# Kernel tuning notes

Hardware: AMD Instinct MI355X
Metric: run time of the kernel (lower is better)

Reference implementation:

```python
import jax, jax.numpy as jnp
import numpy as np

MODEL_DIM = 1024
NUM_EXPERTS = 64
CAPACITY_FACTOR = 1.0
MIN_CAPACITY = 8


def setup_inputs() -> dict:
    key = jax.random.key(0)
    kx, kw = jax.random.split(key)
    x = jax.random.normal(kx, (4, 2048, MODEL_DIM), dtype=jnp.float32)
    wg = jax.random.normal(kw, (MODEL_DIM, NUM_EXPERTS), dtype=jnp.float32) * (1.0 / np.sqrt(MODEL_DIM))
    return {"x": x, "wg": wg}


def reference(x, wg):
    d = x.shape[-1]
    tokens = x.reshape(-1, d)                      # [s, m]
    s = tokens.shape[0]
    e = wg.shape[1]
    # capacity per _capacity(): ceil(num_tokens/num_experts * capacity_factor), floored at min_capacity
    capacity = max(int(np.ceil(s / e * CAPACITY_FACTOR)), MIN_CAPACITY)

    logits = tokens @ wg                           # [s, e]  (wg Linear, no bias)
    gates = jax.nn.softmax(logits, axis=1)         # [s, e]

    indices1_s = jnp.argmax(gates, axis=1)         # [s] top-1 expert per token
    mask1 = jax.nn.one_hot(indices1_s, e, dtype=jnp.int32)  # [s, e]
    exp_counts = jnp.sum(mask1, axis=0)            # [e]

    # load-balancing aux loss
    me = jnp.mean(gates, axis=0)                   # [e]
    ce = jnp.mean(mask1.astype(jnp.float32), axis=0)
    l_aux = jnp.sum(me * ce) * e

    # position of each token within its expert's buffer
    locations1 = jnp.cumsum(mask1, axis=0) - 1     # [s, e]
    locations1_s = jnp.sum(locations1 * mask1, axis=1)  # [s]

    gates_masked = gates * mask1.astype(jnp.float32)    # [s, e]
    # one_hot zeros out indices >= capacity (token dropped)
    locations1_sc = jax.nn.one_hot(locations1_s, capacity, dtype=jnp.float32)  # [s, c]
    combine_weights = jnp.einsum('se,sc->sec', gates_masked, locations1_sc)    # [s, e, c]
    dispatch_mask = combine_weights.astype(bool)
    return (l_aux, combine_weights, dispatch_mask, mask1, exp_counts, indices1_s)
```

## Files before the change

kernel.cpp:

```cpp
#include <hip/hip_runtime.h>
#include <hip/hip_bf16.h>

#define S_TOK 8192
#define NEXP 64
#define MDIM 1024
#define CAP 128
#define BLK_TOK 32
#define NCH 256

#define OFF2 67108865
#define OFF3 134217729
#define OFF4 134742017
#define OFF5 134742081

__global__ __launch_bounds__(256) void gate_kernel(
    const float* __restrict__ x, const float* __restrict__ wg,
    unsigned char* __restrict__ ind, unsigned char* __restrict__ rnk,
    float* __restrict__ gval, unsigned char* __restrict__ counts,
    float* __restrict__ gparts)
{
  __shared__ float wgt[4 * 64 * NEXP];
  __shared__ float g_all[BLK_TOK][NEXP];
  __shared__ int s_ind[BLK_TOK];
  const int b = blockIdx.x;
  const int tid = threadIdx.x;
  const int lane = tid & 63;
  const int wv = tid >> 6;
  const int eg = lane & 15;
  const int tg = lane >> 4;
  const int tokbase = b * BLK_TOK + tg * 8;

  const float4* x4 = reinterpret_cast<const float4*>(x);
  const float4* wg4 = reinterpret_cast<const float4*>(wg);
  float4* wgt4 = reinterpret_cast<float4*>(wgt);

  float4 acc[8];
#pragma unroll
  for (int j = 0; j < 8; ++j) acc[j] = make_float4(0.f, 0.f, 0.f, 0.f);

#pragma unroll
  for (int p = 0; p < 4; ++p) {
    __syncthreads();
#pragma unroll
    for (int k = 0; k < 16; ++k) {
      const int c = k * 256 + tid;
      const int wq = c >> 10;
      const int rem = c & 1023;
      wgt4[c] = wg4[wq * 4096 + p * 1024 + rem];
    }
    __syncthreads();

    const float4* wrow = wgt4 + wv * 1024;
    const int xcol0 = wv * 64 + p * 16;
#pragma unroll 2
    for (int dq = 0; dq < 16; ++dq) {
      const float4 w0 = wrow[(4 * dq + 0) * 16 + eg];
      const float4 w1 = wrow[(4 * dq + 1) * 16 + eg];
      const float4 w2 = wrow[(4 * dq + 2) * 16 + eg];
      const float4 w3 = wrow[(4 * dq + 3) * 16 + eg];
#pragma unroll
      for (int j = 0; j < 8; ++j) {
        const float4 xv = x4[(tokbase + j) * (MDIM / 4) + xcol0 + dq];
        acc[j].x = fmaf(xv.x, w0.x, fmaf(xv.y, w1.x, fmaf(xv.z, w2.x, fmaf(xv.w, w3.x, acc[j].x))));
        acc[j].y = fmaf(xv.x, w0.y, fmaf(xv.y, w1.y, fmaf(xv.z, w2.y, fmaf(xv.w, w3.y, acc[j].y))));
        acc[j].z = fmaf(xv.x, w0.z, fmaf(xv.y, w1.z, fmaf(xv.z, w2.z, fmaf(xv.w, w3.z, acc[j].z))));
        acc[j].w = fmaf(xv.x, w0.w, fmaf(xv.y, w1.w, fmaf(xv.z, w2.w, fmaf(xv.w, w3.w, acc[j].w))));
      }
    }
  }

  __syncthreads();
#pragma unroll
  for (int j = 0; j < 8; ++j)
    wgt4[(wv * BLK_TOK + tg * 8 + j) * 16 + eg] = acc[j];
  __syncthreads();

#pragma unroll
  for (int jj = 0; jj < 2; ++jj) {
    const int tl = wv * 8 + jj * 4 + tg;
    const float4 s0 = wgt4[(0 * BLK_TOK + tl) * 16 + eg];
    const float4 s1 = wgt4[(1 * BLK_TOK + tl) * 16 + eg];
    const float4 s2 = wgt4[(2 * BLK_TOK + tl) * 16 + eg];
    const float4 s3 = wgt4[(3 * BLK_TOK + tl) * 16 + eg];
    const float l0 = s0.x + s1.x + s2.x + s3.x;
    const float l1 = s0.y + s1.y + s2.y + s3.y;
    const float l2 = s0.z + s1.z + s2.z + s3.z;
    const float l3 = s0.w + s1.w + s2.w + s3.w;

    float m = l0; int ei = eg * 4;
    if (l1 > m) { m = l1; ei = eg * 4 + 1; }
    if (l2 > m) { m = l2; ei = eg * 4 + 2; }
    if (l3 > m) { m = l3; ei = eg * 4 + 3; }
#pragma unroll
    for (int off = 1; off <= 8; off <<= 1) {
      const float om = __shfl_xor(m, off, 64);
      const int oe = __shfl_xor(ei, off, 64);
      if (om > m || (om == m && oe < ei)) { m = om; ei = oe; }
    }
    const float e0 = __expf(l0 - m), e1 = __expf(l1 - m),
                e2 = __expf(l2 - m), e3 = __expf(l3 - m);
    float sm = e0 + e1 + e2 + e3;
#pragma unroll
    for (int off = 1; off <= 8; off <<= 1) sm += __shfl_xor(sm, off, 64);
    const float inv = 1.0f / sm;

    *reinterpret_cast<float4*>(&g_all[tl][eg * 4]) =
        make_float4(e0 * inv, e1 * inv, e2 * inv, e3 * inv);
    if (eg == 0) {
      s_ind[tl] = ei;
      const int gt = b * BLK_TOK + tl;
      ind[gt] = (unsigned char)ei;
      gval[gt] = inv;
    }
  }
  __syncthreads();

  if (wv == 0) {
    float colsum = 0.f;
#pragma unroll
    for (int t = 0; t < BLK_TOK; ++t) colsum += g_all[t][lane];
    gparts[b * NEXP + lane] = colsum;
    int cnt = 0;
#pragma unroll
    for (int t = 0; t < BLK_TOK; ++t) {
      const int e = s_ind[t];
      const int r = __shfl(cnt, e, 64);
      if (lane == 0) rnk[b * BLK_TOK + t] = (unsigned char)r;
      cnt += (lane == e) ? 1 : 0;
    }
    counts[b * NEXP + lane] = (unsigned char)cnt;
  }
}

__global__ __launch_bounds__(1024) void reduce_kernel(
    const unsigned char* __restrict__ counts, const float* __restrict__ gparts,
    unsigned short* __restrict__ offs, float* __restrict__ out)
{
  __shared__ int s_cnt[16][64];
  __shared__ float s_gs[16][64];
  const int e = threadIdx.x & 63;
  const int g = threadIdx.x >> 6;
  const int ch0 = g * 16;

  int csum = 0; float gsum = 0.f;
#pragma unroll
  for (int ch = ch0; ch < ch0 + 16; ++ch) {
    csum += (int)counts[ch * NEXP + e];
    gsum += gparts[ch * NEXP + e];
  }
  s_cnt[g][e] = csum; s_gs[g][e] = gsum;
  __syncthreads();

  int base = 0;
  for (int k = 0; k < g; ++k) base += s_cnt[k][e];
  int run = base;
#pragma unroll
  for (int ch = ch0; ch < ch0 + 16; ++ch) {
    offs[ch * NEXP + e] = (unsigned short)run;
    run += (int)counts[ch * NEXP + e];
  }
  if (g == 15) {
    const int total = run;
    out[OFF4 + e] = (float)total;
    float gtot = 0.f;
#pragma unroll
    for (int k = 0; k < 16; ++k) gtot += s_gs[k][e];
    const float me = gtot * (1.0f / (float)S_TOK);
    const float ce = (float)total * (1.0f / (float)S_TOK);
    float prod = me * ce;
#pragma unroll
    for (int off = 32; off > 0; off >>= 1) prod += __shfl_xor(prod, off, 64);
    if (e == 0) out[0] = prod * (float)NEXP;
  }
}

__global__ __launch_bounds__(256) void scatter_kernel(
    const unsigned char* __restrict__ ind, const unsigned char* __restrict__ rnk,
    const unsigned short* __restrict__ offs, const float* __restrict__ gval,
    float* __restrict__ out)
{
  const int s = blockIdx.x * 256 + threadIdx.x;
  if (s >= S_TOK) return;
  const int e = (int)ind[s];
  const int loc = (int)offs[(s >> 5) * NEXP + e] + (int)rnk[s];
  out[OFF5 + s] = (float)e;
  out[OFF3 + (s << 6) + e] = 1.0f;
  if (loc < CAP) {
    const int rel = (s << 13) + (e << 7) + loc;
    out[1 + rel] = gval[s];
    out[OFF2 + rel] = 1.0f;
  }
}

extern "C" void kernel_launch(void* const* d_in, const int* in_sizes, int n_in,
                              void* d_out, int out_size, void* d_ws, size_t ws_size,
                              hipStream_t stream)
{
  const float* x = (const float*)d_in[0];
  const float* wg = (const float*)d_in[1];
  float* out = (float*)d_out;

  float* gval = (float*)d_ws;
  float* gparts = gval + S_TOK;
  unsigned short* offs = (unsigned short*)(gparts + NCH * NEXP);
  unsigned char* ind = (unsigned char*)(offs + NCH * NEXP);
  unsigned char* rnk = ind + S_TOK;
  unsigned char* counts = rnk + S_TOK;

  hipMemsetAsync(out, 0, (size_t)out_size * sizeof(float), stream);
  gate_kernel<<<NCH, 256, 0, stream>>>(x, wg, ind, rnk, gval, counts, gparts);
  reduce_kernel<<<1, 1024, 0, stream>>>(counts, gparts, offs, out);
  scatter_kernel<<<(S_TOK + 255) / 256, 256, 0, stream>>>(ind, rnk, offs, gval, out);
}
```

Before: 134.5 us.

## Fuse output zero-fill into gate kernel and drop LDS staging of gate weights

Replaces the separate hipMemsetAsync with extra zero-fill blocks launched alongside the gating GEMM blocks, so the large output clear overlaps with the logits computation. The gate GEMM is restructured to split the K dimension by wave-free full-row accumulation: each thread computes two tokens over all 1024 dims reading wg directly from global/L2 instead of staging it in LDS, removing the cross-wave partial-sum reduction and barriers. The trade is more global/L2 traffic for wg and less register blocking per thread, and fill blocks compete with gate blocks for CUs.

```diff
diff --git a/kernel.cpp b/kernel.cpp
--- a/kernel.cpp
+++ b/kernel.cpp
@@ -7,103 +7,91 @@
 #define CAP 128
 #define BLK_TOK 32
 #define NCH 256
+#define NGATE 256
+#define NFILL 2048
+#define SLAB 16450
 
 #define OFF2 67108865
 #define OFF3 134217729
 #define OFF4 134742017
 #define OFF5 134742081
-
-__global__ __launch_bounds__(256) void gate_kernel(
+#define OUT_ELEMS 134750273
+#define SLOTS_TOT 33687568
+
+__global__ __launch_bounds__(256) void fused_kernel(
     const float* __restrict__ x, const float* __restrict__ wg,
     unsigned char* __restrict__ ind, unsigned char* __restrict__ rnk,
     float* __restrict__ gval, unsigned char* __restrict__ counts,
-    float* __restrict__ gparts)
-{
-  __shared__ float wgt[4 * 64 * NEXP];
+    float* __restrict__ gparts, float* __restrict__ out)
+{
   __shared__ float g_all[BLK_TOK][NEXP];
   __shared__ int s_ind[BLK_TOK];
   const int b = blockIdx.x;
+
+  if (b >= NGATE) {
+    const long long start = (long long)(b - NGATE) * SLAB;
+    long long end = start + SLAB;
+    if (end > SLOTS_TOT) end = SLOTS_TOT;
+    float4* o4 = reinterpret_cast<float4*>(out);
+    const float4 z = make_float4(0.f, 0.f, 0.f, 0.f);
+    for (long long j = start + threadIdx.x; j < end; j += 256) o4[j] = z;
+    if (b == NGATE && threadIdx.x == 0) out[OUT_ELEMS - 1] = 0.f;
+    return;
+  }
+
   const int tid = threadIdx.x;
   const int lane = tid & 63;
   const int wv = tid >> 6;
   const int eg = lane & 15;
   const int tg = lane >> 4;
-  const int tokbase = b * BLK_TOK + tg * 8;
+  const int t0 = wv * 8 + tg;
+  const int gt0 = b * BLK_TOK + t0;
 
   const float4* x4 = reinterpret_cast<const float4*>(x);
   const float4* wg4 = reinterpret_cast<const float4*>(wg);
-  float4* wgt4 = reinterpret_cast<float4*>(wgt);
-
-  float4 acc[8];
-#pragma unroll
-  for (int j = 0; j < 8; ++j) acc[j] = make_float4(0.f, 0.f, 0.f, 0.f);
-
-#pragma unroll
-  for (int p = 0; p < 4; ++p) {
-    __syncthreads();
-#pragma unroll
-    for (int k = 0; k < 16; ++k) {
-      const int c = k * 256 + tid;
-      const int wq = c >> 10;
-      const int rem = c & 1023;
-      wgt4[c] = wg4[wq * 4096 + p * 1024 + rem];
-    }
-    __syncthreads();
-
-    const float4* wrow = wgt4 + wv * 1024;
-    const int xcol0 = wv * 64 + p * 16;
-#pragma unroll 2
-    for (int dq = 0; dq < 16; ++dq) {
-      const float4 w0 = wrow[(4 * dq + 0) * 16 + eg];
-      const float4 w1 = wrow[(4 * dq + 1) * 16 + eg];
-      const float4 w2 = wrow[(4 * dq + 2) * 16 + eg];
-      const float4 w3 = wrow[(4 * dq + 3) * 16 + eg];
-#pragma unroll
-      for (int j = 0; j < 8; ++j) {
-        const float4 xv = x4[(tokbase + j) * (MDIM / 4) + xcol0 + dq];
-        acc[j].x = fmaf(xv.x, w0.x, fmaf(xv.y, w1.x, fmaf(xv.z, w2.x, fmaf(xv.w, w3.x, acc[j].x))));
-        acc[j].y = fmaf(xv.x, w0.y, fmaf(xv.y, w1.y, fmaf(xv.z, w2.y, fmaf(xv.w, w3.y, acc[j].y))));
-        acc[j].z = fmaf(xv.x, w0.z, fmaf(xv.y, w1.z, fmaf(xv.z, w2.z, fmaf(xv.w, w3.z, acc[j].z))));
-        acc[j].w = fmaf(xv.x, w0.w, fmaf(xv.y, w1.w, fmaf(xv.z, w2.w, fmaf(xv.w, w3.w, acc[j].w))));
-      }
-    }
-  }
-
-  __syncthreads();
-#pragma unroll
-  for (int j = 0; j < 8; ++j)
-    wgt4[(wv * BLK_TOK + tg * 8 + j) * 16 + eg] = acc[j];
-  __syncthreads();
-
-#pragma unroll
-  for (int jj = 0; jj < 2; ++jj) {
-    const int tl = wv * 8 + jj * 4 + tg;
-    const float4 s0 = wgt4[(0 * BLK_TOK + tl) * 16 + eg];
-    const float4 s1 = wgt4[(1 * BLK_TOK + tl) * 16 + eg];
-    const float4 s2 = wgt4[(2 * BLK_TOK + tl) * 16 + eg];
-    const float4 s3 = wgt4[(3 * BLK_TOK + tl) * 16 + eg];
-    const float l0 = s0.x + s1.x + s2.x + s3.x;
-    const float l1 = s0.y + s1.y + s2.y + s3.y;
-    const float l2 = s0.z + s1.z + s2.z + s3.z;
-    const float l3 = s0.w + s1.w + s2.w + s3.w;
-
-    float m = l0; int ei = eg * 4;
-    if (l1 > m) { m = l1; ei = eg * 4 + 1; }
-    if (l2 > m) { m = l2; ei = eg * 4 + 2; }
-    if (l3 > m) { m = l3; ei = eg * 4 + 3; }
+  const float4* xr0 = x4 + (size_t)gt0 * (MDIM / 4);
+  const float4* xr1 = xr0 + (size_t)4 * (MDIM / 4);
+
+  float4 a0 = make_float4(0.f, 0.f, 0.f, 0.f);
+  float4 a1 = make_float4(0.f, 0.f, 0.f, 0.f);
+#pragma unroll 4
+  for (int dq = 0; dq < MDIM / 4; ++dq) {
+    const float4 w0 = wg4[(4 * dq + 0) * 16 + eg];
+    const float4 w1 = wg4[(4 * dq + 1) * 16 + eg];
+    const float4 w2 = wg4[(4 * dq + 2) * 16 + eg];
+    const float4 w3 = wg4[(4 * dq + 3) * 16 + eg];
+    const float4 xv0 = xr0[dq];
+    const float4 xv1 = xr1[dq];
+    a0.x = fmaf(xv0.x, w0.x, fmaf(xv0.y, w1.x, fmaf(xv0.z, w2.x, fmaf(xv0.w, w3.x, a0.x))));
+    a0.y = fmaf(xv0.x, w0.y, fmaf(xv0.y, w1.y, fmaf(xv0.z, w2.y, fmaf(xv0.w, w3.y, a0.y))));
+    a0.z = fmaf(xv0.x, w0.z, fmaf(xv0.y, w1.z, fmaf(xv0.z, w2.z, fmaf(xv0.w, w3.z, a0.z))));
+    a0.w = fmaf(xv0.x, w0.w, fmaf(xv0.y, w1.w, fmaf(xv0.z, w2.w, fmaf(xv0.w, w3.w, a0.w))));
+    a1.x = fmaf(xv1.x, w0.x, fmaf(xv1.y, w1.x, fmaf(xv1.z, w2.x, fmaf(xv1.w, w3.x, a1.x))));
+    a1.y = fmaf(xv1.x, w0.y, fmaf(xv1.y, w1.y, fmaf(xv1.z, w2.y, fmaf(xv1.w, w3.y, a1.y))));
+    a1.z = fmaf(xv1.x, w0.z, fmaf(xv1.y, w1.z, fmaf(xv1.z, w2.z, fmaf(xv1.w, w3.z, a1.z))));
+    a1.w = fmaf(xv1.x, w0.w, fmaf(xv1.y, w1.w, fmaf(xv1.z, w2.w, fmaf(xv1.w, w3.w, a1.w))));
+  }
+
+#pragma unroll
+  for (int half = 0; half < 2; ++half) {
+    const float4 lg = half ? a1 : a0;
+    const int tl = t0 + half * 4;
+    float m = lg.x; int ei = eg * 4;
+    if (lg.y > m) { m = lg.y; ei = eg * 4 + 1; }
+    if (lg.z > m) { m = lg.z; ei = eg * 4 + 2; }
+    if (lg.w > m) { m = lg.w; ei = eg * 4 + 3; }
 #pragma unroll
     for (int off = 1; off <= 8; off <<= 1) {
       const float om = __shfl_xor(m, off, 64);
       const int oe = __shfl_xor(ei, off, 64);
       if (om > m || (om == m && oe < ei)) { m = om; ei = oe; }
     }
-    const float e0 = __expf(l0 - m), e1 = __expf(l1 - m),
-                e2 = __expf(l2 - m), e3 = __expf(l3 - m);
+    const float e0 = __expf(lg.x - m), e1 = __expf(lg.y - m),
+                e2 = __expf(lg.z - m), e3 = __expf(lg.w - m);
     float sm = e0 + e1 + e2 + e3;
 #pragma unroll
     for (int off = 1; off <= 8; off <<= 1) sm += __shfl_xor(sm, off, 64);
     const float inv = 1.0f / sm;
-
     *reinterpret_cast<float4*>(&g_all[tl][eg * 4]) =
         make_float4(e0 * inv, e1 * inv, e2 * inv, e3 * inv);
     if (eg == 0) {
@@ -207,8 +195,7 @@
   unsigned char* rnk = ind + S_TOK;
   unsigned char* counts = rnk + S_TOK;
 
-  hipMemsetAsync(out, 0, (size_t)out_size * sizeof(float), stream);
-  gate_kernel<<<NCH, 256, 0, stream>>>(x, wg, ind, rnk, gval, counts, gparts);
+  fused_kernel<<<NGATE + NFILL, 256, 0, stream>>>(x, wg, ind, rnk, gval, counts, gparts, out);
   reduce_kernel<<<1, 1024, 0, stream>>>(counts, gparts, offs, out);
   scatter_kernel<<<(S_TOK + 255) / 256, 256, 0, stream>>>(ind, rnk, offs, gval, out);
 }
```

Measured after the change: 220.3 us. 63.8% more time.
